# Performance work log

Hardware: AMD Instinct MI355X
Metric: run time of the kernel (lower is better)

The kernel has to match this reference:

```python
import jax, jax.numpy as jnp
import numpy as np

ALPHA = 0.8
B = 32768

def setup_inputs() -> dict:
    key = jax.random.key(0)
    ks = jax.random.split(key, 18)
    def w(k, shape, fan_in):
        return (jax.random.normal(k, shape, dtype=jnp.float32) / np.sqrt(fan_in)).astype(jnp.float32)
    return {
        "f1_norm": jax.random.normal(ks[0], (B, 1, 768), dtype=jnp.float32),
        "f2_norm": jax.random.normal(ks[1], (B, 1, 600), dtype=jnp.float32),
        "W_enc1": w(ks[2], (64, 768), 768), "b_enc1": jnp.zeros((64,), jnp.float32),
        "W_enc2": w(ks[3], (64, 600), 600), "b_enc2": jnp.zeros((64,), jnp.float32),
        "W_aff_a": w(ks[4], (8, 2), 2), "W_aff_v": w(ks[5], (8, 2), 2),
        "W_a": w(ks[6], (32, 64), 64), "W_v": w(ks[7], (32, 64), 64),
        "W_ca": w(ks[8], (32, 8), 8), "W_cv": w(ks[9], (32, 8), 8),
        "W_ha": w(ks[10], (8, 32), 32), "W_hv": w(ks[11], (8, 32), 32),
        "W_r1": w(ks[12], (128, 1024), 1024), "b_r1": jnp.zeros((128,), jnp.float32),
        "W_r2": w(ks[13], (32, 128), 128), "b_r2": jnp.zeros((32,), jnp.float32),
    }

def reference(f1_norm, f2_norm, W_enc1, b_enc1, W_enc2, b_enc2,
              W_aff_a, W_aff_v, W_a, W_v, W_ca, W_cv, W_ha, W_hv,
              W_r1, b_r1, W_r2, b_r2):
    # Batched version of the per-sample loop. Per-sample: imu_fts [1,64], vis_fts [1,64].
    imu = f1_norm @ W_enc1.T + b_enc1            # [B,1,64]
    vis = f2_norm @ W_enc2.T + b_enc2            # [B,1,64]
    ivT = jnp.swapaxes(jnp.concatenate([imu, vis], axis=1), 1, 2)  # [B,64,2]
    a_t = ivT @ W_aff_a.T                        # [B,64,8]
    v_t = ivT @ W_aff_v.T                        # [B,64,8]
    scale = jnp.asarray(1.0 / 8.0, dtype=imu.dtype)  # 1/sqrt(64)
    imu_att = jnp.tanh((imu @ a_t) * scale)      # [B,1,8]
    vis_att = jnp.tanh((vis @ v_t) * scale)      # [B,1,8]
    H_a = jax.nn.relu(ALPHA * (imu_att @ W_ca.T + imu @ W_a.T))          # [B,1,32]
    H_v = jax.nn.relu((1.0 - ALPHA) * (vis_att @ W_cv.T + vis @ W_v.T))  # [B,1,32]
    # [B,8,1] + [B,1,64] broadcasts to [B,8,64] (matches torch broadcast in the loop)
    att_imu = ALPHA * jnp.swapaxes(H_a @ W_ha.T, 1, 2) + imu             # [B,8,64]
    att_vis = (1.0 - ALPHA) * jnp.swapaxes(H_v @ W_hv.T, 1, 2) + vis     # [B,8,64]
    feats = jnp.concatenate([att_imu, att_vis], axis=2).reshape(f1_norm.shape[0], 1024)
    h = feats @ W_r1.T + b_r1                    # [B,128]  (dropout = identity in eval)
    return h @ W_r2.T + b_r2                     # [B,32]
```

## Files before the change

kernel.cpp:

```cpp
#include <hip/hip_runtime.h>
#include <hip/hip_bf16.h>

#define ALPHA 0.8f
#define SPB 64
#define IVW 132

typedef __attribute__((ext_vector_type(8))) short bf16x8;
typedef __attribute__((ext_vector_type(8))) unsigned short ushort8;
typedef __attribute__((ext_vector_type(4))) unsigned short ushort4v;
typedef __attribute__((ext_vector_type(4))) float f32x4;

__device__ __forceinline__ unsigned short bfu(float x) {
    __hip_bfloat16 h = __float2bfloat16(x);
    return __builtin_bit_cast(unsigned short, h);
}
__device__ __forceinline__ float b2f(unsigned short u) {
    return __builtin_bit_cast(float, ((unsigned)u) << 16);
}

__global__ void prepA(const float* __restrict__ Wr1, float* __restrict__ M) {
    int idx = blockIdx.x * 256 + threadIdx.x;
    if (idx >= 144 * 128) return;
    int x = idx >> 7;
    int r = idx & 127;
    const float* row = Wr1 + (size_t)r * 1024;
    float s = 0.f;
    if (x < 64) {
        #pragma unroll
        for (int j = 0; j < 8; ++j) s += row[j * 128 + x];
    } else if (x < 128) {
        #pragma unroll
        for (int j = 0; j < 8; ++j) s += row[j * 128 + 64 + (x - 64)];
    } else if (x < 136) {
        int j = x - 128;
        for (int k = 0; k < 64; ++k) s += row[j * 128 + k];
    } else {
        int j = x - 136;
        for (int k = 0; k < 64; ++k) s += row[j * 128 + 64 + k];
    }
    M[x * 128 + r] = s;
}

__global__ void prepB(const float* __restrict__ M, const float* __restrict__ Wr2,
                      const float* __restrict__ br1, const float* __restrict__ br2,
                      float* __restrict__ G, float* __restrict__ c) {
    int idx = blockIdx.x * 256 + threadIdx.x;
    if (idx < 144 * 32) {
        int x = idx >> 5, o = idx & 31;
        const float* m = M + x * 128;
        const float* w = Wr2 + o * 128;
        float s = 0.f;
        for (int r = 0; r < 128; ++r) s = fmaf(m[r], w[r], s);
        G[x * 32 + o] = s;
    } else if (idx < 144 * 32 + 32) {
        int o = idx - 144 * 32;
        const float* w = Wr2 + o * 128;
        float s = br2[o];
        for (int r = 0; r < 128; ++r) s = fmaf(br1[r], w[r], s);
        c[o] = s;
    }
}

__global__ void prepWf(const float* __restrict__ We1, const float* __restrict__ We2,
                       unsigned short* __restrict__ Wf1, unsigned short* __restrict__ Wf2) {
    int idx = blockIdx.x * 256 + threadIdx.x;
    if (idx >= 11264) return;
    const bool e2 = idx >= 6144;
    const int f = e2 ? idx - 6144 : idx;
    const int lane = f & 63, frag = f >> 6;
    const int nt = frag & 3, ks = frag >> 2;
    const int row = nt * 16 + (lane & 15);
    const int k0 = ks * 32 + (lane >> 4) * 8;
    ushort8 v;
    if (!e2) {
        const float* wr = We1 + (size_t)row * 768 + k0;
        #pragma unroll
        for (int e = 0; e < 8; ++e) v[e] = bfu(wr[e]);
        *(ushort8*)(Wf1 + (size_t)frag * 512 + lane * 8) = v;
    } else {
        #pragma unroll
        for (int e = 0; e < 8; ++e) {
            const int k = k0 + e;
            v[e] = (k < 600) ? bfu(We2[(size_t)row * 600 + k]) : (unsigned short)0;
        }
        *(ushort8*)(Wf2 + (size_t)frag * 512 + lane * 8) = v;
    }
}

template <int KLEN, int NWIN>
__device__ __forceinline__ void encW(const float* __restrict__ X,
                                     const unsigned short* __restrict__ Wf,
                                     const float* __restrict__ bias,
                                     unsigned short* __restrict__ lds,
                                     unsigned short* __restrict__ ivb,
                                     int colbase, int s0w, int l) {
    const int r16 = l & 15, kg = l >> 4;
    const int srow = l >> 5;
    const int q = l & 31;
    const int ch = q >> 1, hh = q & 1;

    f32x4 acc0 = {0.f,0.f,0.f,0.f}, acc1 = {0.f,0.f,0.f,0.f};
    f32x4 acc2 = {0.f,0.f,0.f,0.f}, acc3 = {0.f,0.f,0.f,0.f};
    f32x4 rv[8];

    #pragma unroll
    for (int j = 0; j < 8; ++j) {
        const int row = 2 * j + srow;
        rv[j] = *(const f32x4*)(X + (size_t)(s0w + row) * KLEN + 4 * q);
    }

    #pragma unroll
    for (int wnd = 0; wnd < NWIN; ++wnd) {
        unsigned short* buf = lds + (wnd & 1) * 2048;
        #pragma unroll
        for (int j = 0; j < 8; ++j) {
            const int row = 2 * j + srow;
            ushort4v pk;
            pk[0] = bfu(rv[j][0]); pk[1] = bfu(rv[j][1]);
            pk[2] = bfu(rv[j][2]); pk[3] = bfu(rv[j][3]);
            *(ushort4v*)((char*)buf + row * 256 +
                         ((ch & 8) | ((ch & 7) ^ (row & 7))) * 16 + hh * 8) = pk;
        }
        if (wnd + 1 < NWIN) {
            const int kb1 = (wnd + 1) * 128;
            #pragma unroll
            for (int j = 0; j < 8; ++j) {
                const int row = 2 * j + srow;
                if (KLEN % 128 == 0 || kb1 + 4 * q + 4 <= KLEN) {
                    rv[j] = *(const f32x4*)(X + (size_t)(s0w + row) * KLEN + kb1 + 4 * q);
                } else {
                    f32x4 z = {0.f,0.f,0.f,0.f};
                    rv[j] = z;
                }
            }
        }
        const unsigned short* wfw = Wf + (size_t)wnd * 16 * 512 + l * 8;
        bf16x8 bb[16];
        #pragma unroll
        for (int i = 0; i < 16; ++i) bb[i] = *(const bf16x8*)(wfw + i * 512);
        #pragma unroll
        for (int kk = 0; kk < 4; ++kk) {
            const int cc = kk * 4 + kg;
            const bf16x8 af = *(const bf16x8*)((const char*)buf + r16 * 256 +
                                 ((cc & 8) | ((cc & 7) ^ (r16 & 7))) * 16);
            acc0 = __builtin_amdgcn_mfma_f32_16x16x32_bf16(af, bb[kk * 4 + 0], acc0, 0, 0, 0);
            acc1 = __builtin_amdgcn_mfma_f32_16x16x32_bf16(af, bb[kk * 4 + 1], acc1, 0, 0, 0);
            acc2 = __builtin_amdgcn_mfma_f32_16x16x32_bf16(af, bb[kk * 4 + 2], acc2, 0, 0, 0);
            acc3 = __builtin_amdgcn_mfma_f32_16x16x32_bf16(af, bb[kk * 4 + 3], acc3, 0, 0, 0);
        }
    }

    const float bz0 = bias[r16], bz1 = bias[16 + r16], bz2 = bias[32 + r16], bz3 = bias[48 + r16];
    const int rr = 4 * kg;
    #pragma unroll
    for (int reg = 0; reg < 4; ++reg) {
        const size_t base = (size_t)(s0w + rr + reg) * 128 + colbase;
        ivb[base +  0 + r16] = bfu(acc0[reg] + bz0);
        ivb[base + 16 + r16] = bfu(acc1[reg] + bz1);
        ivb[base + 32 + r16] = bfu(acc2[reg] + bz2);
        ivb[base + 48 + r16] = bfu(acc3[reg] + bz3);
    }
}

__global__ __launch_bounds__(256)
void mica_enc(const float* __restrict__ f1, const float* __restrict__ f2,
              const unsigned short* __restrict__ Wf1, const unsigned short* __restrict__ Wf2,
              const float* __restrict__ be1, const float* __restrict__ be2,
              unsigned short* __restrict__ ivb) {
    __shared__ __align__(16) unsigned short lds[4 * 2 * 2048];
    const int t = threadIdx.x;
    const int w = t >> 6, l = t & 63;
    unsigned short* ldsw = lds + w * 4096;
    const int s0w = blockIdx.x * SPB + w * 16;
    encW<768, 6>(f1, Wf1, be1, ldsw, ivb, 0,  s0w, l);
    encW<600, 5>(f2, Wf2, be2, ldsw, ivb, 64, s0w, l);
}

__global__ __launch_bounds__(256, 2)
void mica_tail(const unsigned short* __restrict__ ivb,
               const float* __restrict__ Waffa, const float* __restrict__ Waffv,
               const float* __restrict__ Wa, const float* __restrict__ Wv,
               const float* __restrict__ Wca, const float* __restrict__ Wcv,
               const float* __restrict__ Wha, const float* __restrict__ Whv,
               const float* __restrict__ G, const float* __restrict__ cvec,
               float* __restrict__ out) {
    __shared__ float sIV[SPB * IVW];
    __shared__ float red[4096];
    const int t = threadIdx.x;
    const int s0 = blockIdx.x * SPB;

    {
        const int row = t & 63, cb = (t >> 6) * 32;
        const unsigned short* src = ivb + (size_t)(s0 + row) * 128 + cb;
        #pragma unroll
        for (int j = 0; j < 4; ++j) {
            const ushort8 v = *(const ushort8*)(src + j * 8);
            f32x4 f0 = {b2f(v[0]), b2f(v[1]), b2f(v[2]), b2f(v[3])};
            f32x4 f1 = {b2f(v[4]), b2f(v[5]), b2f(v[6]), b2f(v[7])};
            *(f32x4*)(sIV + row * IVW + cb + j * 8)     = f0;
            *(f32x4*)(sIV + row * IVW + cb + j * 8 + 4) = f1;
        }
    }
    __syncthreads();

    const int s = t & 63;
    const int q = t >> 6;
    const float* iv = sIV + s * IVW;

    float sii = 0.f, siv = 0.f, svv = 0.f;
    #pragma unroll
    for (int h = 0; h < 2; ++h) {
        const f32x4 a0 = *(const f32x4*)(iv + q * 16 + h * 8);
        const f32x4 a1 = *(const f32x4*)(iv + q * 16 + h * 8 + 4);
        const f32x4 b0 = *(const f32x4*)(iv + 64 + q * 16 + h * 8);
        const f32x4 b1 = *(const f32x4*)(iv + 64 + q * 16 + h * 8 + 4);
        #pragma unroll
        for (int j = 0; j < 4; ++j) {
            sii = fmaf(a0[j], a0[j], sii); siv = fmaf(a0[j], b0[j], siv); svv = fmaf(b0[j], b0[j], svv);
            sii = fmaf(a1[j], a1[j], sii); siv = fmaf(a1[j], b1[j], siv); svv = fmaf(b1[j], b1[j], svv);
        }
    }
    red[(q * 3 + 0) * 64 + s] = sii;
    red[(q * 3 + 1) * 64 + s] = siv;
    red[(q * 3 + 2) * 64 + s] = svv;
    __syncthreads();
    sii = 0.f; siv = 0.f; svv = 0.f;
    #pragma unroll
    for (int g = 0; g < 4; ++g) {
        sii += red[(g * 3 + 0) * 64 + s];
        siv += red[(g * 3 + 1) * 64 + s];
        svv += red[(g * 3 + 2) * 64 + s];
    }

    float ia[8], va[8];
    #pragma unroll
    for (int j = 0; j < 8; ++j) {
        ia[j] = tanhf((sii * Waffa[j * 2 + 0] + siv * Waffa[j * 2 + 1]) * 0.125f);
        va[j] = tanhf((siv * Waffv[j * 2 + 0] + svv * Waffv[j * 2 + 1]) * 0.125f);
    }

    float Ha[8], Hv[8];
    #pragma unroll
    for (int mi = 0; mi < 8; ++mi) {
        const int m = q * 8 + mi;
        float sa = 0.f, sv = 0.f;
        #pragma unroll
        for (int j = 0; j < 8; ++j) {
            sa = fmaf(ia[j], Wca[m * 8 + j], sa);
            sv = fmaf(va[j], Wcv[m * 8 + j], sv);
        }
        Ha[mi] = sa; Hv[mi] = sv;
    }
    for (int k4 = 0; k4 < 64; k4 += 4) {
        const f32x4 a4 = *(const f32x4*)(iv + k4);
        const f32x4 b4 = *(const f32x4*)(iv + 64 + k4);
        #pragma unroll
        for (int mi = 0; mi < 8; ++mi) {
            const int m = q * 8 + mi;
            const f32x4 wa = *(const f32x4*)(Wa + m * 64 + k4);
            const f32x4 wv = *(const f32x4*)(Wv + m * 64 + k4);
            #pragma unroll
            for (int j = 0; j < 4; ++j) {
                Ha[mi] = fmaf(a4[j], wa[j], Ha[mi]);
                Hv[mi] = fmaf(b4[j], wv[j], Hv[mi]);
            }
        }
    }
    #pragma unroll
    for (int mi = 0; mi < 8; ++mi) {
        Ha[mi] = fmaxf(ALPHA * Ha[mi], 0.f);
        Hv[mi] = fmaxf((1.f - ALPHA) * Hv[mi], 0.f);
    }

    __syncthreads();

    #pragma unroll
    for (int j = 0; j < 8; ++j) {
        float hap = 0.f, hvp = 0.f;
        #pragma unroll
        for (int mi = 0; mi < 8; ++mi) {
            hap = fmaf(Ha[mi], Wha[j * 32 + q * 8 + mi], hap);
            hvp = fmaf(Hv[mi], Whv[j * 32 + q * 8 + mi], hvp);
        }
        red[(q * 16 + j) * 64 + s] = hap;
        red[(q * 16 + 8 + j) * 64 + s] = hvp;
    }
    __syncthreads();
    float ha[8], hv[8];
    #pragma unroll
    for (int j = 0; j < 8; ++j) {
        float sa = 0.f, sv = 0.f;
        #pragma unroll
        for (int g = 0; g < 4; ++g) {
            sa += red[(g * 16 + j) * 64 + s];
            sv += red[(g * 16 + 8 + j) * 64 + s];
        }
        ha[j] = sa; hv[j] = sv;
    }

    float o8[8];
    #pragma unroll
    for (int oi = 0; oi < 8; ++oi) o8[oi] = cvec[q * 8 + oi];
    for (int k4 = 0; k4 < 128; k4 += 4) {
        const f32x4 a4 = *(const f32x4*)(iv + k4);
        #pragma unroll
        for (int kk = 0; kk < 4; ++kk) {
            const f32x4 g0 = *(const f32x4*)(G + (k4 + kk) * 32 + q * 8);
            const f32x4 g1 = *(const f32x4*)(G + (k4 + kk) * 32 + q * 8 + 4);
            #pragma unroll
            for (int oi = 0; oi < 4; ++oi) {
                o8[oi]     = fmaf(a4[kk], g0[oi], o8[oi]);
                o8[4 + oi] = fmaf(a4[kk], g1[oi], o8[4 + oi]);
            }
        }
    }
    #pragma unroll
    for (int j = 0; j < 8; ++j) {
        const float aj = ALPHA * ha[j];
        const float vj = (1.f - ALPHA) * hv[j];
        const f32x4 ga0 = *(const f32x4*)(G + (128 + j) * 32 + q * 8);
        const f32x4 ga1 = *(const f32x4*)(G + (128 + j) * 32 + q * 8 + 4);
        const f32x4 gv0 = *(const f32x4*)(G + (136 + j) * 32 + q * 8);
        const f32x4 gv1 = *(const f32x4*)(G + (136 + j) * 32 + q * 8 + 4);
        #pragma unroll
        for (int oi = 0; oi < 4; ++oi) {
            o8[oi]     = fmaf(aj, ga0[oi], o8[oi]);
            o8[4 + oi] = fmaf(aj, ga1[oi], o8[4 + oi]);
            o8[oi]     = fmaf(vj, gv0[oi], o8[oi]);
            o8[4 + oi] = fmaf(vj, gv1[oi], o8[4 + oi]);
        }
    }
    f32x4 v0 = {o8[0], o8[1], o8[2], o8[3]};
    f32x4 v1 = {o8[4], o8[5], o8[6], o8[7]};
    float* op = out + (size_t)(s0 + s) * 32 + q * 8;
    *(f32x4*)op = v0;
    *((f32x4*)op + 1) = v1;
}

extern "C" void kernel_launch(void* const* d_in, const int* in_sizes, int n_in,
                              void* d_out, int out_size, void* d_ws, size_t ws_size,
                              hipStream_t stream) {
    const float* f1    = (const float*)d_in[0];
    const float* f2    = (const float*)d_in[1];
    const float* We1   = (const float*)d_in[2];
    const float* be1   = (const float*)d_in[3];
    const float* We2   = (const float*)d_in[4];
    const float* be2   = (const float*)d_in[5];
    const float* Waffa = (const float*)d_in[6];
    const float* Waffv = (const float*)d_in[7];
    const float* Wa    = (const float*)d_in[8];
    const float* Wv    = (const float*)d_in[9];
    const float* Wca   = (const float*)d_in[10];
    const float* Wcv   = (const float*)d_in[11];
    const float* Wha   = (const float*)d_in[12];
    const float* Whv   = (const float*)d_in[13];
    const float* Wr1   = (const float*)d_in[14];
    const float* br1   = (const float*)d_in[15];
    const float* Wr2   = (const float*)d_in[16];
    const float* br2   = (const float*)d_in[17];
    float* outp = (float*)d_out;

    const int Btot = in_sizes[0] / 768;

    float* M = (float*)d_ws;
    float* G = (float*)((char*)d_ws + 73728);
    float* c = (float*)((char*)d_ws + 92160);
    unsigned short* Wf1 = (unsigned short*)((char*)d_ws + 92288);
    unsigned short* Wf2 = (unsigned short*)((char*)d_ws + 190592);
    unsigned short* ivb = (unsigned short*)((char*)d_ws + 272512);

    prepA<<<(144 * 128 + 255) / 256, 256, 0, stream>>>(Wr1, M);
    prepB<<<(144 * 32 + 32 + 255) / 256, 256, 0, stream>>>(M, Wr2, br1, br2, G, c);
    prepWf<<<44, 256, 0, stream>>>(We1, We2, Wf1, Wf2);
    mica_enc<<<Btot / SPB, 256, 0, stream>>>(f1, f2, Wf1, Wf2, be1, be2, ivb);
    mica_tail<<<Btot / SPB, 256, 0, stream>>>(ivb, Waffa, Waffv, Wa, Wv,
                                              Wca, Wcv, Wha, Whv, G, c, outp);
}
```

Before: 88.26 us.

## Split encoder K dimension across waves with LDS reduction, 16 samples per block

The encoder kernel now has each block handle 16 samples instead of 64. Its four waves split the K dimension into quarters (split-K), and partial MFMA accumulators are reduced through shared memory by wave 0. This raises the grid size fourfold and shrinks per-wave register use (launch bounds 256,6), aiming for more occupancy and memory parallelism on the bandwidth-bound input read. The cost is extra syncthreads, LDS reduction traffic, and reloading the full weight fragments in every block.

Result: no change. 89.85 us (+1.8%).

```diff
diff --git a/kernel.cpp b/kernel.cpp
--- a/kernel.cpp
+++ b/kernel.cpp
@@ -87,93 +87,116 @@
     }
 }
 
-template <int KLEN, int NWIN>
-__device__ __forceinline__ void encW(const float* __restrict__ X,
+template <int KLEN, int CQ>
+__device__ __forceinline__ void encQ(const float* __restrict__ X,
                                      const unsigned short* __restrict__ Wf,
                                      const float* __restrict__ bias,
-                                     unsigned short* __restrict__ lds,
+                                     unsigned short* __restrict__ sbuf,
+                                     float* __restrict__ sred,
                                      unsigned short* __restrict__ ivb,
-                                     int colbase, int s0w, int l) {
+                                     int colbase, int s0, int kq, int l) {
     const int r16 = l & 15, kg = l >> 4;
-    const int srow = l >> 5;
-    const int q = l & 31;
-    const int ch = q >> 1, hh = q & 1;
+    const int sr = l >> 3, q = l & 7;
+    const int base_ks = kq * CQ;
 
     f32x4 acc0 = {0.f,0.f,0.f,0.f}, acc1 = {0.f,0.f,0.f,0.f};
     f32x4 acc2 = {0.f,0.f,0.f,0.f}, acc3 = {0.f,0.f,0.f,0.f};
-    f32x4 rv[8];
-
-    #pragma unroll
-    for (int j = 0; j < 8; ++j) {
-        const int row = 2 * j + srow;
-        rv[j] = *(const f32x4*)(X + (size_t)(s0w + row) * KLEN + 4 * q);
-    }
-
-    #pragma unroll
-    for (int wnd = 0; wnd < NWIN; ++wnd) {
-        unsigned short* buf = lds + (wnd & 1) * 2048;
-        #pragma unroll
-        for (int j = 0; j < 8; ++j) {
-            const int row = 2 * j + srow;
-            ushort4v pk;
-            pk[0] = bfu(rv[j][0]); pk[1] = bfu(rv[j][1]);
-            pk[2] = bfu(rv[j][2]); pk[3] = bfu(rv[j][3]);
-            *(ushort4v*)((char*)buf + row * 256 +
-                         ((ch & 8) | ((ch & 7) ^ (row & 7))) * 16 + hh * 8) = pk;
-        }
-        if (wnd + 1 < NWIN) {
-            const int kb1 = (wnd + 1) * 128;
+    f32x4 rv0, rv1;
+
+    {
+        const int kb = base_ks * 32 + 4 * q;
+        if (KLEN % 32 == 0 || kb + 4 <= KLEN) {
+            rv0 = *(const f32x4*)(X + (size_t)(s0 + sr) * KLEN + kb);
+            rv1 = *(const f32x4*)(X + (size_t)(s0 + 8 + sr) * KLEN + kb);
+        } else {
+            f32x4 z = {0.f,0.f,0.f,0.f};
+            rv0 = z; rv1 = z;
+        }
+    }
+
+    #pragma unroll
+    for (int wnd = 0; wnd < CQ; ++wnd) {
+        const int ks = base_ks + wnd;
+        unsigned short* buf = sbuf + (wnd & 1) * 512;
+        {
+            ushort4v p0, p1;
+            p0[0] = bfu(rv0[0]); p0[1] = bfu(rv0[1]); p0[2] = bfu(rv0[2]); p0[3] = bfu(rv0[3]);
+            p1[0] = bfu(rv1[0]); p1[1] = bfu(rv1[1]); p1[2] = bfu(rv1[2]); p1[3] = bfu(rv1[3]);
+            *(ushort4v*)(buf + sr * 32 + q * 4)       = p0;
+            *(ushort4v*)(buf + (8 + sr) * 32 + q * 4) = p1;
+        }
+        if (wnd + 1 < CQ) {
+            const int kb = (ks + 1) * 32 + 4 * q;
+            if (KLEN % 32 == 0 || kb + 4 <= KLEN) {
+                rv0 = *(const f32x4*)(X + (size_t)(s0 + sr) * KLEN + kb);
+                rv1 = *(const f32x4*)(X + (size_t)(s0 + 8 + sr) * KLEN + kb);
+            } else {
+                f32x4 z = {0.f,0.f,0.f,0.f};
+                rv0 = z; rv1 = z;
+            }
+        }
+        const unsigned short* wfp = Wf + (size_t)(ks * 4) * 512 + l * 8;
+        const bf16x8 b0 = *(const bf16x8*)(wfp);
+        const bf16x8 b1 = *(const bf16x8*)(wfp + 512);
+        const bf16x8 b2 = *(const bf16x8*)(wfp + 1024);
+        const bf16x8 b3 = *(const bf16x8*)(wfp + 1536);
+        const bf16x8 af = *(const bf16x8*)(buf + r16 * 32 + kg * 8);
+        acc0 = __builtin_amdgcn_mfma_f32_16x16x32_bf16(af, b0, acc0, 0, 0, 0);
+        acc1 = __builtin_amdgcn_mfma_f32_16x16x32_bf16(af, b1, acc1, 0, 0, 0);
+        acc2 = __builtin_amdgcn_mfma_f32_16x16x32_bf16(af, b2, acc2, 0, 0, 0);
+        acc3 = __builtin_amdgcn_mfma_f32_16x16x32_bf16(af, b3, acc3, 0, 0, 0);
+    }
+
+    __syncthreads();
+    if (kq != 0) {
+        float* dst = sred + (size_t)(kq - 1) * 1024;
+        #pragma unroll
+        for (int reg = 0; reg < 4; ++reg) {
+            dst[(0 * 4 + reg) * 64 + l] = acc0[reg];
+            dst[(1 * 4 + reg) * 64 + l] = acc1[reg];
+            dst[(2 * 4 + reg) * 64 + l] = acc2[reg];
+            dst[(3 * 4 + reg) * 64 + l] = acc3[reg];
+        }
+    }
+    __syncthreads();
+    if (kq == 0) {
+        #pragma unroll
+        for (int g = 0; g < 3; ++g) {
+            const float* srcp = sred + (size_t)g * 1024;
             #pragma unroll
-            for (int j = 0; j < 8; ++j) {
-                const int row = 2 * j + srow;
-                if (KLEN % 128 == 0 || kb1 + 4 * q + 4 <= KLEN) {
-                    rv[j] = *(const f32x4*)(X + (size_t)(s0w + row) * KLEN + kb1 + 4 * q);
-                } else {
-                    f32x4 z = {0.f,0.f,0.f,0.f};
-                    rv[j] = z;
-                }
+            for (int reg = 0; reg < 4; ++reg) {
+                acc0[reg] += srcp[(0 * 4 + reg) * 64 + l];
+                acc1[reg] += srcp[(1 * 4 + reg) * 64 + l];
+                acc2[reg] += srcp[(2 * 4 + reg) * 64 + l];
+                acc3[reg] += srcp[(3 * 4 + reg) * 64 + l];
             }
         }
-        const unsigned short* wfw = Wf + (size_t)wnd * 16 * 512 + l * 8;
-        bf16x8 bb[16];
-        #pragma unroll
-        for (int i = 0; i < 16; ++i) bb[i] = *(const bf16x8*)(wfw + i * 512);
-        #pragma unroll
-        for (int kk = 0; kk < 4; ++kk) {
-            const int cc = kk * 4 + kg;
-            const bf16x8 af = *(const bf16x8*)((const char*)buf + r16 * 256 +
-                                 ((cc & 8) | ((cc & 7) ^ (r16 & 7))) * 16);
-            acc0 = __builtin_amdgcn_mfma_f32_16x16x32_bf16(af, bb[kk * 4 + 0], acc0, 0, 0, 0);
-            acc1 = __builtin_amdgcn_mfma_f32_16x16x32_bf16(af, bb[kk * 4 + 1], acc1, 0, 0, 0);
-            acc2 = __builtin_amdgcn_mfma_f32_16x16x32_bf16(af, bb[kk * 4 + 2], acc2, 0, 0, 0);
-            acc3 = __builtin_amdgcn_mfma_f32_16x16x32_bf16(af, bb[kk * 4 + 3], acc3, 0, 0, 0);
-        }
-    }
-
-    const float bz0 = bias[r16], bz1 = bias[16 + r16], bz2 = bias[32 + r16], bz3 = bias[48 + r16];
-    const int rr = 4 * kg;
-    #pragma unroll
-    for (int reg = 0; reg < 4; ++reg) {
-        const size_t base = (size_t)(s0w + rr + reg) * 128 + colbase;
-        ivb[base +  0 + r16] = bfu(acc0[reg] + bz0);
-        ivb[base + 16 + r16] = bfu(acc1[reg] + bz1);
-        ivb[base + 32 + r16] = bfu(acc2[reg] + bz2);
-        ivb[base + 48 + r16] = bfu(acc3[reg] + bz3);
-    }
-}
-
-__global__ __launch_bounds__(256)
+        const float bz0 = bias[r16], bz1 = bias[16 + r16], bz2 = bias[32 + r16], bz3 = bias[48 + r16];
+        const int rr = 4 * kg;
+        #pragma unroll
+        for (int reg = 0; reg < 4; ++reg) {
+            const size_t base = (size_t)(s0 + rr + reg) * 128 + colbase;
+            ivb[base +  0 + r16] = bfu(acc0[reg] + bz0);
+            ivb[base + 16 + r16] = bfu(acc1[reg] + bz1);
+            ivb[base + 32 + r16] = bfu(acc2[reg] + bz2);
+            ivb[base + 48 + r16] = bfu(acc3[reg] + bz3);
+        }
+    }
+}
+
+__global__ __launch_bounds__(256, 6)
 void mica_enc(const float* __restrict__ f1, const float* __restrict__ f2,
               const unsigned short* __restrict__ Wf1, const unsigned short* __restrict__ Wf2,
               const float* __restrict__ be1, const float* __restrict__ be2,
               unsigned short* __restrict__ ivb) {
-    __shared__ __align__(16) unsigned short lds[4 * 2 * 2048];
+    __shared__ __align__(16) unsigned short sstage[4 * 1024];
+    __shared__ float sred[3 * 1024];
     const int t = threadIdx.x;
-    const int w = t >> 6, l = t & 63;
-    unsigned short* ldsw = lds + w * 4096;
-    const int s0w = blockIdx.x * SPB + w * 16;
-    encW<768, 6>(f1, Wf1, be1, ldsw, ivb, 0,  s0w, l);
-    encW<600, 5>(f2, Wf2, be2, ldsw, ivb, 64, s0w, l);
+    const int kq = t >> 6, l = t & 63;
+    unsigned short* sbuf = sstage + kq * 1024;
+    const int s0 = blockIdx.x * 16;
+    encQ<768, 6>(f1, Wf1, be1, sbuf, sred, ivb, 0,  s0, kq, l);
+    encQ<600, 5>(f2, Wf2, be2, sbuf, sred, ivb, 64, s0, kq, l);
 }
 
 __global__ __launch_bounds__(256, 2)
@@ -372,7 +395,7 @@
     prepA<<<(144 * 128 + 255) / 256, 256, 0, stream>>>(Wr1, M);
     prepB<<<(144 * 32 + 32 + 255) / 256, 256, 0, stream>>>(M, Wr2, br1, br2, G, c);
     prepWf<<<44, 256, 0, stream>>>(We1, We2, Wf1, Wf2);
-    mica_enc<<<Btot / SPB, 256, 0, stream>>>(f1, f2, Wf1, Wf2, be1, be2, ivb);
+    mica_enc<<<Btot / 16, 256, 0, stream>>>(f1, f2, Wf1, Wf2, be1, be2, ivb);
     mica_tail<<<Btot / SPB, 256, 0, stream>>>(ivb, Waffa, Waffv, Wa, Wv,
                                               Wca, Wcv, Wha, Whv, G, c, outp);
 }
```

## Restructure encoder GEMM to share weight tiles in LDS across eight waves

Applied to the files above, without the earlier changes.

The encoder kernel now uses 512-thread blocks covering 128 samples. Each encoder weight chunk is staged once into shared memory and reused by all eight waves, instead of every wave reading the bf16 weight fragments from global memory. Input rows are streamed in 32-wide K steps through a three-deep register prefetch and a double-buffered swizzled LDS tile. Both encoders' weights are padded to 96 fragments so the 600-wide encoder runs the same three-chunk loop. This aims to cut global weight traffic and improve latency hiding, at the cost of block-wide syncs, wasted MMA work on the padded K range, and higher LDS use per block.

Result: no change. 90.01 us (+2.0%).

```diff
diff --git a/kernel.cpp b/kernel.cpp
--- a/kernel.cpp
+++ b/kernel.cpp
@@ -64,9 +64,9 @@
 __global__ void prepWf(const float* __restrict__ We1, const float* __restrict__ We2,
                        unsigned short* __restrict__ Wf1, unsigned short* __restrict__ Wf2) {
     int idx = blockIdx.x * 256 + threadIdx.x;
-    if (idx >= 11264) return;
-    const bool e2 = idx >= 6144;
-    const int f = e2 ? idx - 6144 : idx;
+    if (idx >= 2 * 96 * 64) return;
+    const bool e2 = idx >= 96 * 64;
+    const int f = e2 ? idx - 96 * 64 : idx;
     const int lane = f & 63, frag = f >> 6;
     const int nt = frag & 3, ks = frag >> 2;
     const int row = nt * 16 + (lane & 15);
@@ -87,74 +87,93 @@
     }
 }
 
-template <int KLEN, int NWIN>
-__device__ __forceinline__ void encW(const float* __restrict__ X,
+template <int KLEN>
+__device__ __forceinline__ void encC(const float* __restrict__ X,
                                      const unsigned short* __restrict__ Wf,
                                      const float* __restrict__ bias,
-                                     unsigned short* __restrict__ lds,
+                                     unsigned short* __restrict__ sB,
+                                     unsigned short* __restrict__ sA,
                                      unsigned short* __restrict__ ivb,
-                                     int colbase, int s0w, int l) {
+                                     int colbase, int s0, int w, int l, int t) {
     const int r16 = l & 15, kg = l >> 4;
-    const int srow = l >> 5;
-    const int q = l & 31;
-    const int ch = q >> 1, hh = q & 1;
+    const int rA = l >> 3;
+    const int g  = l & 7;
+    const int rowbase = s0 + w * 16;
 
     f32x4 acc0 = {0.f,0.f,0.f,0.f}, acc1 = {0.f,0.f,0.f,0.f};
     f32x4 acc2 = {0.f,0.f,0.f,0.f}, acc3 = {0.f,0.f,0.f,0.f};
-    f32x4 rv[8];
-
-    #pragma unroll
-    for (int j = 0; j < 8; ++j) {
-        const int row = 2 * j + srow;
-        rv[j] = *(const f32x4*)(X + (size_t)(s0w + row) * KLEN + 4 * q);
-    }
-
-    #pragma unroll
-    for (int wnd = 0; wnd < NWIN; ++wnd) {
-        unsigned short* buf = lds + (wnd & 1) * 2048;
-        #pragma unroll
-        for (int j = 0; j < 8; ++j) {
-            const int row = 2 * j + srow;
-            ushort4v pk;
-            pk[0] = bfu(rv[j][0]); pk[1] = bfu(rv[j][1]);
-            pk[2] = bfu(rv[j][2]); pk[3] = bfu(rv[j][3]);
-            *(ushort4v*)((char*)buf + row * 256 +
-                         ((ch & 8) | ((ch & 7) ^ (row & 7))) * 16 + hh * 8) = pk;
-        }
-        if (wnd + 1 < NWIN) {
-            const int kb1 = (wnd + 1) * 128;
+    f32x4 rv[3][2];
+
+    #define LOADA(KST, DST)                                                        \
+        {                                                                          \
+            const int k0_ = (KST) * 32 + g * 4;                                    \
+            _Pragma("unroll")                                                      \
+            for (int j_ = 0; j_ < 2; ++j_) {                                       \
+                const int row_ = j_ * 8 + rA;                                      \
+                if (KLEN % 32 == 0 || k0_ + 4 <= KLEN) {                           \
+                    DST[j_] = *(const f32x4*)(X + (size_t)(rowbase + row_) * KLEN + k0_); \
+                } else {                                                           \
+                    f32x4 z_ = {0.f,0.f,0.f,0.f};                                  \
+                    DST[j_] = z_;                                                  \
+                }                                                                  \
+            }                                                                      \
+        }
+    #define WRITEA(KST, SRC)                                                       \
+        {                                                                          \
+            unsigned short* buf_ = sA + ((KST) & 1) * 512;                         \
+            _Pragma("unroll")                                                      \
+            for (int j_ = 0; j_ < 2; ++j_) {                                       \
+                const int row_ = j_ * 8 + rA;                                      \
+                ushort4v p_;                                                       \
+                p_[0] = bfu(SRC[j_][0]); p_[1] = bfu(SRC[j_][1]);                  \
+                p_[2] = bfu(SRC[j_][2]); p_[3] = bfu(SRC[j_][3]);                  \
+                *(ushort4v*)(buf_ + row_ * 32 +                                    \
+                    (((g >> 1) ^ ((row_ >> 1) & 3)) << 3) + ((g & 1) << 2)) = p_;  \
+            }                                                                      \
+        }
+
+    LOADA(0, rv[0]); LOADA(1, rv[1]); LOADA(2, rv[2]);
+
+    #pragma unroll
+    for (int q = 0; q < 3; ++q) {
+        __syncthreads();
+        {
+            const unsigned short* src = Wf + (size_t)q * 16384;
             #pragma unroll
-            for (int j = 0; j < 8; ++j) {
-                const int row = 2 * j + srow;
-                if (KLEN % 128 == 0 || kb1 + 4 * q + 4 <= KLEN) {
-                    rv[j] = *(const f32x4*)(X + (size_t)(s0w + row) * KLEN + kb1 + 4 * q);
-                } else {
-                    f32x4 z = {0.f,0.f,0.f,0.f};
-                    rv[j] = z;
-                }
+            for (int p = 0; p < 4; ++p) {
+                const int u = p * 512 + t;
+                *(ushort8*)(sB + u * 8) = *(const ushort8*)(src + u * 8);
             }
         }
-        const unsigned short* wfw = Wf + (size_t)wnd * 16 * 512 + l * 8;
-        bf16x8 bb[16];
-        #pragma unroll
-        for (int i = 0; i < 16; ++i) bb[i] = *(const bf16x8*)(wfw + i * 512);
-        #pragma unroll
-        for (int kk = 0; kk < 4; ++kk) {
-            const int cc = kk * 4 + kg;
-            const bf16x8 af = *(const bf16x8*)((const char*)buf + r16 * 256 +
-                                 ((cc & 8) | ((cc & 7) ^ (r16 & 7))) * 16);
-            acc0 = __builtin_amdgcn_mfma_f32_16x16x32_bf16(af, bb[kk * 4 + 0], acc0, 0, 0, 0);
-            acc1 = __builtin_amdgcn_mfma_f32_16x16x32_bf16(af, bb[kk * 4 + 1], acc1, 0, 0, 0);
-            acc2 = __builtin_amdgcn_mfma_f32_16x16x32_bf16(af, bb[kk * 4 + 2], acc2, 0, 0, 0);
-            acc3 = __builtin_amdgcn_mfma_f32_16x16x32_bf16(af, bb[kk * 4 + 3], acc3, 0, 0, 0);
-        }
-    }
+        __syncthreads();
+        if (q == 0) { WRITEA(0, rv[0]); }
+        #pragma unroll
+        for (int ks = 0; ks < 8; ++ks) {
+            const int kst = q * 8 + ks;
+            if (kst + 3 < 24) { LOADA(kst + 3, rv[(kst + 3) % 3]); }
+            if (kst + 1 < 24) { WRITEA(kst + 1, rv[(kst + 1) % 3]); }
+            const unsigned short* bb = sB + (ks * 4) * 512 + l * 8;
+            const bf16x8 b0 = *(const bf16x8*)(bb);
+            const bf16x8 b1 = *(const bf16x8*)(bb + 512);
+            const bf16x8 b2 = *(const bf16x8*)(bb + 1024);
+            const bf16x8 b3 = *(const bf16x8*)(bb + 1536);
+            const unsigned short* abuf = sA + (kst & 1) * 512;
+            const bf16x8 af = *(const bf16x8*)(abuf + r16 * 32 +
+                                ((kg ^ ((r16 >> 1) & 3)) << 3));
+            acc0 = __builtin_amdgcn_mfma_f32_16x16x32_bf16(af, b0, acc0, 0, 0, 0);
+            acc1 = __builtin_amdgcn_mfma_f32_16x16x32_bf16(af, b1, acc1, 0, 0, 0);
+            acc2 = __builtin_amdgcn_mfma_f32_16x16x32_bf16(af, b2, acc2, 0, 0, 0);
+            acc3 = __builtin_amdgcn_mfma_f32_16x16x32_bf16(af, b3, acc3, 0, 0, 0);
+        }
+    }
+    #undef LOADA
+    #undef WRITEA
 
     const float bz0 = bias[r16], bz1 = bias[16 + r16], bz2 = bias[32 + r16], bz3 = bias[48 + r16];
     const int rr = 4 * kg;
     #pragma unroll
     for (int reg = 0; reg < 4; ++reg) {
-        const size_t base = (size_t)(s0w + rr + reg) * 128 + colbase;
+        const size_t base = (size_t)(rowbase + rr + reg) * 128 + colbase;
         ivb[base +  0 + r16] = bfu(acc0[reg] + bz0);
         ivb[base + 16 + r16] = bfu(acc1[reg] + bz1);
         ivb[base + 32 + r16] = bfu(acc2[reg] + bz2);
@@ -162,18 +181,19 @@
     }
 }
 
-__global__ __launch_bounds__(256)
+__global__ __launch_bounds__(512, 2)
 void mica_enc(const float* __restrict__ f1, const float* __restrict__ f2,
               const unsigned short* __restrict__ Wf1, const unsigned short* __restrict__ Wf2,
               const float* __restrict__ be1, const float* __restrict__ be2,
               unsigned short* __restrict__ ivb) {
-    __shared__ __align__(16) unsigned short lds[4 * 2 * 2048];
+    __shared__ __align__(16) unsigned short sB[16384];
+    __shared__ __align__(16) unsigned short sA[8 * 1024];
     const int t = threadIdx.x;
     const int w = t >> 6, l = t & 63;
-    unsigned short* ldsw = lds + w * 4096;
-    const int s0w = blockIdx.x * SPB + w * 16;
-    encW<768, 6>(f1, Wf1, be1, ldsw, ivb, 0,  s0w, l);
-    encW<600, 5>(f2, Wf2, be2, ldsw, ivb, 64, s0w, l);
+    unsigned short* sAw = sA + w * 1024;
+    const int s0 = blockIdx.x * 128;
+    encC<768>(f1, Wf1, be1, sB, sAw, ivb, 0,  s0, w, l, t);
+    encC<600>(f2, Wf2, be2, sB, sAw, ivb, 64, s0, w, l, t);
 }
 
 __global__ __launch_bounds__(256, 2)
@@ -367,12 +387,12 @@
     float* c = (float*)((char*)d_ws + 92160);
     unsigned short* Wf1 = (unsigned short*)((char*)d_ws + 92288);
     unsigned short* Wf2 = (unsigned short*)((char*)d_ws + 190592);
-    unsigned short* ivb = (unsigned short*)((char*)d_ws + 272512);
+    unsigned short* ivb = (unsigned short*)((char*)d_ws + 288896);
 
     prepA<<<(144 * 128 + 255) / 256, 256, 0, stream>>>(Wr1, M);
     prepB<<<(144 * 32 + 32 + 255) / 256, 256, 0, stream>>>(M, Wr2, br1, br2, G, c);
-    prepWf<<<44, 256, 0, stream>>>(We1, We2, Wf1, Wf2);
-    mica_enc<<<Btot / SPB, 256, 0, stream>>>(f1, f2, Wf1, Wf2, be1, be2, ivb);
+    prepWf<<<48, 256, 0, stream>>>(We1, We2, Wf1, Wf2);
+    mica_enc<<<Btot / 128, 512, 0, stream>>>(f1, f2, Wf1, Wf2, be1, be2, ivb);
     mica_tail<<<Btot / SPB, 256, 0, stream>>>(ivb, Waffa, Waffv, Wa, Wv,
                                               Wca, Wcv, Wha, Whv, G, c, outp);
 }
```
